# Performance work log

Measured on AMD Instinct MI355X. Metric: run time of the kernel, lower is better.

The kernel has to match this reference:

```python
import jax, jax.numpy as jnp
import numpy as np
from jax import lax

V, E, H, L, B, T = 32000, 300, 512, 17, 32, 256


def _lstm_dir(x, w_ih, w_hh, b_ih, b_hh):
    # x: [B,T,E]; torch gate order i,f,g,o stacked in 4H
    Bn = x.shape[0]
    xg = jnp.einsum('bte,ge->btg', x, w_ih) + b_ih + b_hh  # [B,T,4H]
    h0 = jnp.zeros((Bn, H), x.dtype)
    c0 = jnp.zeros((Bn, H), x.dtype)

    def step(carry, xg_t):
        h, c = carry
        g = xg_t + h @ w_hh.T
        i, f, gg, o = jnp.split(g, 4, axis=-1)
        i = jax.nn.sigmoid(i)
        f = jax.nn.sigmoid(f)
        gg = jnp.tanh(gg)
        o = jax.nn.sigmoid(o)
        c = f * c + i * gg
        h = o * jnp.tanh(c)
        return (h, c), h

    _, hs = lax.scan(step, (h0, c0), jnp.swapaxes(xg, 0, 1))
    return jnp.swapaxes(hs, 0, 1)  # [B,T,H]


def _forward(input_ids, labels, mask, emb, w_ih_f, w_hh_f, b_ih_f, b_hh_f,
             w_ih_b, w_hh_b, b_ih_b, b_hh_b, w_cls, b_cls,
             start_trans, end_trans, trans):
    x = emb[input_ids]                                   # [B,T,E]
    hf = _lstm_dir(x, w_ih_f, w_hh_f, b_ih_f, b_hh_f)
    hb = _lstm_dir(x[:, ::-1], w_ih_b, w_hh_b, b_ih_b, b_hh_b)[:, ::-1]
    h = jnp.concatenate([hf, hb], axis=-1)               # [B,T,2H]
    em = h @ w_cls.T + b_cls                             # [B,T,L] emissions

    # ---- CRF log-likelihood (torchcrf semantics), time-major ----
    em_t = jnp.swapaxes(em, 0, 1)                        # [T,B,L]
    tags = jnp.swapaxes(labels, 0, 1)                    # [T,B]
    m = jnp.swapaxes(mask, 0, 1).astype(em.dtype)        # [T,B]
    barange = jnp.arange(em.shape[0])

    # numerator: score of gold path
    score = start_trans[tags[0]] + em_t[0, barange, tags[0]]

    def num_step(s, inp):
        e_t, tp, tt, mt = inp
        return s + mt * (trans[tp, tt] + e_t[barange, tt]), None

    score, _ = lax.scan(num_step, score, (em_t[1:], tags[:-1], tags[1:], m[1:]))
    seq_ends = jnp.sum(m, axis=0).astype(jnp.int32) - 1
    last_tags = tags[seq_ends, barange]
    score = score + end_trans[last_tags]

    # denominator: forward algorithm (log partition)
    alpha = start_trans + em_t[0]                        # [B,L]

    def den_step(a, inp):
        e_t, mt = inp
        nxt = jax.nn.logsumexp(a[:, :, None] + trans[None, :, :] + e_t[:, None, :], axis=1)
        return jnp.where(mt[:, None] > 0, nxt, a), None

    alpha, _ = lax.scan(den_step, alpha, (em_t[1:], m[1:]))
    logZ = jax.nn.logsumexp(alpha + end_trans, axis=-1)

    llh = score - logZ                                   # [B]
    return -jnp.mean(llh)                                # reduction='mean', loss = -llh


def setup_inputs():
    key = jax.random.key(0)
    ks = jax.random.split(key, 16)
    s = 1.0 / np.sqrt(H)
    s2 = 1.0 / np.sqrt(2 * H)
    u = lambda k, shp, sc: jax.random.uniform(k, shp, jnp.float32, -sc, sc)
    emb = jax.random.normal(ks[0], (V, E), jnp.float32)
    emb = emb.at[0].set(0.0)  # padding_idx=0 row zeroed
    return {
        'input_ids': jax.random.randint(ks[1], (B, T), 0, V, jnp.int32),
        'labels': jax.random.randint(ks[2], (B, T), 0, L, jnp.int32),
        'mask': jnp.ones((B, T), bool),
        'emb': emb,
        'w_ih_f': u(ks[3], (4 * H, E), s), 'w_hh_f': u(ks[4], (4 * H, H), s),
        'b_ih_f': u(ks[5], (4 * H,), s), 'b_hh_f': u(ks[6], (4 * H,), s),
        'w_ih_b': u(ks[7], (4 * H, E), s), 'w_hh_b': u(ks[8], (4 * H, H), s),
        'b_ih_b': u(ks[9], (4 * H,), s), 'b_hh_b': u(ks[10], (4 * H,), s),
        'w_cls': u(ks[11], (L, 2 * H), s2), 'b_cls': u(ks[12], (L,), s2),
        'start_trans': u(ks[13], (L,), 0.1),
        'end_trans': u(ks[14], (L,), 0.1),
        'trans': u(ks[15], (L, L), 0.1),
    }


def reference(input_ids, labels, mask, emb, w_ih_f, w_hh_f, b_ih_f, b_hh_f,
              w_ih_b, w_hh_b, b_ih_b, b_hh_b, w_cls, b_cls,
              start_trans, end_trans, trans):
    return _forward(input_ids, labels, mask, emb, w_ih_f, w_hh_f, b_ih_f, b_hh_f,
                    w_ih_b, w_hh_b, b_ih_b, b_hh_b, w_cls, b_cls,
                    start_trans, end_trans, trans)
```

## Files before the change

### kernel.cpp

```cpp
#include <hip/hip_runtime.h>

#define TT 256
#define BB 32
#define HH 512
#define EE 300
#define LL 17
#define G4 2048

#define NGRP 16

using u16 = unsigned short;
using u32 = unsigned int;
using u64 = unsigned long long;

typedef _Float16 half8 __attribute__((ext_vector_type(8)));
typedef short bf16x8 __attribute__((ext_vector_type(8)));
typedef float f32x4 __attribute__((ext_vector_type(4)));

__device__ __forceinline__ u32 f2bf(float f) {
  u32 u = __float_as_uint(f);
  return (u + 0x7FFFu + ((u >> 16) & 1u)) >> 16;
}
__device__ __forceinline__ float bfbits2f(u32 lo) { return __uint_as_float(lo << 16); }

__device__ __forceinline__ u32 pkf16(float a, float b) {
  u16 lo = __builtin_bit_cast(u16, (_Float16)a);
  u16 hi = __builtin_bit_cast(u16, (_Float16)b);
  return (u32)lo | ((u32)hi << 16);
}
__device__ __forceinline__ float f16lo(u32 p) {
  return (float)__builtin_bit_cast(_Float16, (u16)(p & 0xFFFFu));
}
__device__ __forceinline__ float f16hi(u32 p) {
  return (float)__builtin_bit_cast(_Float16, (u16)(p >> 16));
}

#define RX __ATOMIC_RELAXED
#define SCA __HIP_MEMORY_SCOPE_AGENT

__global__ __launch_bounds__(256) void k_zero(u64* __restrict__ hx64) {
  int i = blockIdx.x * 256 + threadIdx.x;
  if (i < 2 * NGRP * 1024) hx64[i] = 0ull;
}

__global__ __launch_bounds__(256) void k_pack4(
    const float* __restrict__ whhf, const float* __restrict__ whhb,
    uint4* __restrict__ wpk2)
{
  int g = blockIdx.x * 256 + threadIdx.x;
  int l = g & 63;
  int kstep = (g >> 6) & 15;
  int t = (g >> 10) & 3;
  int js = (g >> 12) & 31;
  int dir = (g >> 17) & 1;
  int r = l & 15;
  int jl = 4 * t + (r >> 2), gate = r & 3;
  int grow = gate * 512 + js * 16 + jl;
  int k0 = kstep * 32 + (l >> 4) * 8;
  const float* wsrc = (dir ? whhb : whhf) + (long)grow * HH + k0;
  uint4 o;
  o.x = pkf16(wsrc[0], wsrc[1]);
  o.y = pkf16(wsrc[2], wsrc[3]);
  o.z = pkf16(wsrc[4], wsrc[5]);
  o.w = pkf16(wsrc[6], wsrc[7]);
  wpk2[g] = o;
}

__global__ __launch_bounds__(256) void k_input_gemm2(
    const int* __restrict__ ids, const float* __restrict__ emb,
    const float* __restrict__ wih_f, const float* __restrict__ wih_b,
    const float* __restrict__ bih_f, const float* __restrict__ bhh_f,
    const float* __restrict__ bih_b, const float* __restrict__ bhh_b,
    u16* __restrict__ xgf, u16* __restrict__ xgb)
{
  __shared__ u32 As[128 * 20];
  __shared__ u32 Bs[128 * 20];
  __shared__ int idl[128];

  const int tid = threadIdx.x;
  const int mb = blockIdx.x & 63;
  const int nb = blockIdx.x >> 6;
  const int m0 = mb * 128;
  const int dir = nb >> 4;
  const int gl0 = (nb & 15) * 128;
  const float* __restrict__ wih = dir ? wih_b : wih_f;

  if (tid < 128) {
    int tk = m0 + tid;
    idl[tid] = ids[(tk & 31) * TT + (tk >> 5)];
  }
  __syncthreads();

  const int w = tid >> 6, l = tid & 63;
  const int lr = l & 15, lq = l >> 4;
  const int sm = tid >> 1, shalf = tid & 1;

  f32x4 acc[2][8];
#pragma unroll
  for (int mi = 0; mi < 2; ++mi)
#pragma unroll
    for (int ni = 0; ni < 8; ++ni) acc[mi][ni] = (f32x4){0.f, 0.f, 0.f, 0.f};

  for (int kc = 0; kc < 10; ++kc) {
    const int kg = kc * 32 + shalf * 16;
    {
      const float* src = emb + (long)idl[sm] * EE;
      u32 pk[8];
#pragma unroll
      for (int j4 = 0; j4 < 4; ++j4) {
        int k = kg + 4 * j4;
        float f0, f1, f2, f3;
        if (k + 3 < EE) {
          float4 v = *(const float4*)(src + k);
          f0 = v.x; f1 = v.y; f2 = v.z; f3 = v.w;
        } else {
          f0 = (k < EE) ? src[k] : 0.f;
          f1 = (k + 1 < EE) ? src[k + 1] : 0.f;
          f2 = (k + 2 < EE) ? src[k + 2] : 0.f;
          f3 = (k + 3 < EE) ? src[k + 3] : 0.f;
        }
        pk[2 * j4] = f2bf(f0) | (f2bf(f1) << 16);
        pk[2 * j4 + 1] = f2bf(f2) | (f2bf(f3) << 16);
      }
      *(uint4*)&As[sm * 20 + shalf * 8] = make_uint4(pk[0], pk[1], pk[2], pk[3]);
      *(uint4*)&As[sm * 20 + shalf * 8 + 4] = make_uint4(pk[4], pk[5], pk[6], pk[7]);
    }
    {
      const float* src = wih + (long)(gl0 + sm) * EE;
      u32 pk[8];
#pragma unroll
      for (int j4 = 0; j4 < 4; ++j4) {
        int k = kg + 4 * j4;
        float f0, f1, f2, f3;
        if (k + 3 < EE) {
          float4 v = *(const float4*)(src + k);
          f0 = v.x; f1 = v.y; f2 = v.z; f3 = v.w;
        } else {
          f0 = (k < EE) ? src[k] : 0.f;
          f1 = (k + 1 < EE) ? src[k + 1] : 0.f;
          f2 = (k + 2 < EE) ? src[k + 2] : 0.f;
          f3 = (k + 3 < EE) ? src[k + 3] : 0.f;
        }
        pk[2 * j4] = f2bf(f0) | (f2bf(f1) << 16);
        pk[2 * j4 + 1] = f2bf(f2) | (f2bf(f3) << 16);
      }
      *(uint4*)&Bs[sm * 20 + shalf * 8] = make_uint4(pk[0], pk[1], pk[2], pk[3]);
      *(uint4*)&Bs[sm * 20 + shalf * 8 + 4] = make_uint4(pk[4], pk[5], pk[6], pk[7]);
    }
    __syncthreads();

    bf16x8 Af[2];
#pragma unroll
    for (int mi = 0; mi < 2; ++mi)
      Af[mi] = __builtin_bit_cast(
          bf16x8, *(const uint4*)&As[(w * 32 + mi * 16 + lr) * 20 + lq * 4]);
#pragma unroll
    for (int ni = 0; ni < 8; ++ni) {
      bf16x8 Bf = __builtin_bit_cast(
          bf16x8, *(const uint4*)&Bs[(ni * 16 + lr) * 20 + lq * 4]);
      acc[0][ni] = __builtin_amdgcn_mfma_f32_16x16x32_bf16(Af[0], Bf, acc[0][ni], 0, 0, 0);
      acc[1][ni] = __builtin_amdgcn_mfma_f32_16x16x32_bf16(Af[1], Bf, acc[1][ni], 0, 0, 0);
    }
    __syncthreads();
  }

  const float* __restrict__ bih = dir ? bih_b : bih_f;
  const float* __restrict__ bhh = dir ? bhh_b : bhh_f;
  u16* __restrict__ xg = dir ? xgb : xgf;
  float bias[8];
#pragma unroll
  for (int ni = 0; ni < 8; ++ni) {
    int g = gl0 + ni * 16 + lr;
    bias[ni] = bih[g] + bhh[g];
  }
#pragma unroll
  for (int mi = 0; mi < 2; ++mi)
#pragma unroll
    for (int ni = 0; ni < 8; ++ni)
#pragma unroll
      for (int r = 0; r < 4; ++r) {
        int tk = m0 + w * 32 + mi * 16 + lq * 4 + r;
        xg[(long)tk * G4 + gl0 + ni * 16 + lr] = (u16)f2bf(acc[mi][ni][r] + bias[ni]);
      }
}

__global__ __launch_bounds__(256, 1) void k_lstm15(
    const u16* __restrict__ xgf, const u16* __restrict__ xgb,
    const uint4* __restrict__ wpk2,
    u64* __restrict__ hx64,
    u32* __restrict__ hsf32, u32* __restrict__ hsb32)
{
  __shared__ uint4 cB[2][2][256];

  const int tid = threadIdx.x;
  const int bx = blockIdx.x;
  const int bg = bx & 7;
  const int js = bx >> 3;

  const int dh = tid >> 7;
  const int u = tid & 127;
  const int wv = (tid >> 6) & 1;
  const int l = tid & 63;
  const int grp = dh * 8 + bg;

  const u16* __restrict__ xg = dh ? xgb : xgf;
  u32* __restrict__ hs32 = dh ? hsb32 : hsf32;

  const int ub = l & 15;
  const bool ubv = ub < 4;
  const int bread = (l >> 4) * 4 + (ub & 3);
  const int jl0 = 8 * wv + (l >> 4);

  half8 A0[16], A1[16];
  {
    const uint4* ap = wpk2 + ((long)dh << 17) + ((long)js << 12) +
                      ((2 * wv) << 10) + l;
#pragma unroll
    for (int ks = 0; ks < 16; ++ks) {
      A0[ks] = __builtin_bit_cast(half8, ap[ks << 6]);
      A1[ks] = __builtin_bit_cast(half8, ap[1024 + (ks << 6)]);
    }
  }

  {
    uint4* c = &cB[0][0][0];
    for (int i = tid; i < 1024; i += 256) c[i] = make_uint4(0u, 0u, 0u, 0u);
  }
  __syncthreads();

  float cs0 = 0.f, cs1 = 0.f;

  for (int s = 0; s < TT; ++s) {
    const int tok = dh ? (TT - 1 - s) : s;

    u32 xq0[4] = {0, 0, 0, 0}, xq1[4] = {0, 0, 0, 0};
    if (ubv) {
      const u16* p = xg + ((long)(tok * BB + bg * 4 + ub) << 11) + js * 16 + jl0;
      xq0[0] = p[0]; xq0[1] = p[512]; xq0[2] = p[1024]; xq0[3] = p[1536];
      const u16* q = p + 4;
      xq1[0] = q[0]; xq1[1] = q[512]; xq1[2] = q[1024]; xq1[3] = q[1536];
    }

    if (s > 0) {
      const u64* hp = hx64 + ((long)(((s - 1) & 1) * NGRP + grp) << 10) + 8 * u;
      const u32 want = (u32)s;
      u64 v0, v1, v2, v3, v4, v5, v6, v7;
      for (;;) {
        v0 = __hip_atomic_load(hp + 0, RX, SCA);
        v1 = __hip_atomic_load(hp + 1, RX, SCA);
        v2 = __hip_atomic_load(hp + 2, RX, SCA);
        v3 = __hip_atomic_load(hp + 3, RX, SCA);
        v4 = __hip_atomic_load(hp + 4, RX, SCA);
        v5 = __hip_atomic_load(hp + 5, RX, SCA);
        v6 = __hip_atomic_load(hp + 6, RX, SCA);
        v7 = __hip_atomic_load(hp + 7, RX, SCA);
        bool ok = ((u32)(v0 >> 32) == want) & ((u32)(v1 >> 32) == want) &
                  ((u32)(v2 >> 32) == want) & ((u32)(v3 >> 32) == want) &
                  ((u32)(v4 >> 32) == want) & ((u32)(v5 >> 32) == want) &
                  ((u32)(v6 >> 32) == want) & ((u32)(v7 >> 32) == want);
        if (ok) break;
        __builtin_amdgcn_s_sleep(1);
      }
      const int par = s & 1;
      const int i0 = 2 * u, i1 = 2 * u + 1;
      const int pk0 = (i0 >> 2) & 15;
      const int e0 = (pk0 * 16 + (i0 & 3) * 4 + (i0 >> 6)) ^ (pk0 & 7);
      const int e1 = (pk0 * 16 + (i1 & 3) * 4 + (i1 >> 6)) ^ (pk0 & 7);
      cB[dh][par][e0] = make_uint4((u32)v0, (u32)v1, (u32)v2, (u32)v3);
      cB[dh][par][e1] = make_uint4((u32)v4, (u32)v5, (u32)v6, (u32)v7);
    }
    __syncthreads();

    f32x4 acc0 = {0.f, 0.f, 0.f, 0.f}, acc1 = {0.f, 0.f, 0.f, 0.f};
    {
      const uint4* cb = &cB[dh][s & 1][0];
#pragma unroll
      for (int ks = 0; ks < 16; ++ks) {
        half8 B = __builtin_bit_cast(half8, cb[(ks * 16 + bread) ^ (ks & 7)]);
        acc0 = __builtin_amdgcn_mfma_f32_16x16x32_f16(A0[ks], B, acc0, 0, 0, 0);
        acc1 = __builtin_amdgcn_mfma_f32_16x16x32_f16(A1[ks], B, acc1, 0, 0, 0);
      }
    }

    {
      float hv = 0.f;
      if (ubv) {
        float y0 = acc0[0] + bfbits2f(xq0[0]);
        float y1 = acc0[1] + bfbits2f(xq0[1]);
        float y2 = acc0[2] + bfbits2f(xq0[2]);
        float y3 = acc0[3] + bfbits2f(xq0[3]);
        float i_ = 1.f / (1.f + __expf(-y0));
        float f_ = 1.f / (1.f + __expf(-y1));
        float gc = fminf(fmaxf(y2, -15.f), 15.f);
        float eg = __expf(2.f * gc);
        float g_ = (eg - 1.f) / (eg + 1.f);
        float o_ = 1.f / (1.f + __expf(-y3));
        cs0 = f_ * cs0 + i_ * g_;
        float cc = fminf(fmaxf(cs0, -15.f), 15.f);
        float ec = __expf(2.f * cc);
        hv = o_ * (ec - 1.f) / (ec + 1.f);
      }
      float hnb = __shfl_down(hv, 16);
      if (ubv && !((l >> 4) & 1)) {
        u32 pr = pkf16(hv, hnb);
        int jp = js * 8 + 4 * wv + ((l >> 4) >> 1);
        __hip_atomic_store(hs32 + ((long)(tok * BB + bg * 4 + ub) << 8) + jp,
                           pr, RX, SCA);
        u64 v = ((u64)(u32)(s + 1) << 32) | (u64)pr;
        __hip_atomic_store(hx64 + ((long)((s & 1) * NGRP + grp) << 10) +
                               ub * 256 + jp, v, RX, SCA);
      }
    }
    {
      float hv = 0.f;
      if (ubv) {
        float y0 = acc1[0] + bfbits2f(xq1[0]);
        float y1 = acc1[1] + bfbits2f(xq1[1]);
        float y2 = acc1[2] + bfbits2f(xq1[2]);
        float y3 = acc1[3] + bfbits2f(xq1[3]);
        float i_ = 1.f / (1.f + __expf(-y0));
        float f_ = 1.f / (1.f + __expf(-y1));
        float gc = fminf(fmaxf(y2, -15.f), 15.f);
        float eg = __expf(2.f * gc);
        float g_ = (eg - 1.f) / (eg + 1.f);
        float o_ = 1.f / (1.f + __expf(-y3));
        cs1 = f_ * cs1 + i_ * g_;
        float cc = fminf(fmaxf(cs1, -15.f), 15.f);
        float ec = __expf(2.f * cc);
        hv = o_ * (ec - 1.f) / (ec + 1.f);
      }
      float hnb = __shfl_down(hv, 16);
      if (ubv && !((l >> 4) & 1)) {
        u32 pr = pkf16(hv, hnb);
        int jp = js * 8 + 4 * wv + 2 + ((l >> 4) >> 1);
        __hip_atomic_store(hs32 + ((long)(tok * BB + bg * 4 + ub) << 8) + jp,
                           pr, RX, SCA);
        u64 v = ((u64)(u32)(s + 1) << 32) | (u64)pr;
        __hip_atomic_store(hx64 + ((long)((s & 1) * NGRP + grp) << 10) +
                               ub * 256 + jp, v, RX, SCA);
      }
    }
  }
}

__global__ __launch_bounds__(128) void k_cls(
    const u32* __restrict__ hsf32, const u32* __restrict__ hsb32,
    const float* __restrict__ wcls, const float* __restrict__ bcls,
    float* __restrict__ em)
{
  __shared__ float h_l[1024];
  __shared__ float part[17][4];
  const int tk = blockIdx.x;
  const int tid = threadIdx.x;

  {
    uint2 vf = ((const uint2*)(hsf32 + (long)tk * 256))[tid];
    uint2 vb = ((const uint2*)(hsb32 + (long)tk * 256))[tid];
    h_l[4 * tid + 0] = f16lo(vf.x); h_l[4 * tid + 1] = f16hi(vf.x);
    h_l[4 * tid + 2] = f16lo(vf.y); h_l[4 * tid + 3] = f16hi(vf.y);
    h_l[512 + 4 * tid + 0] = f16lo(vb.x); h_l[512 + 4 * tid + 1] = f16hi(vb.x);
    h_l[512 + 4 * tid + 2] = f16lo(vb.y); h_l[512 + 4 * tid + 3] = f16hi(vb.y);
  }
  __syncthreads();

  if (tid < 68) {
    const int ll = tid >> 2, kq = tid & 3;
    const float4* wr = (const float4*)(wcls + (long)ll * 1024 + kq * 256);
    const float4* hr = (const float4*)(h_l + kq * 256);
    float sum = 0.f;
#pragma unroll 4
    for (int i = 0; i < 64; ++i) {
      float4 a = hr[i]; float4 wv = wr[i];
      sum += a.x * wv.x + a.y * wv.y + a.z * wv.z + a.w * wv.w;
    }
    part[ll][kq] = sum;
  }
  __syncthreads();
  if (tid < LL) {
    float v = bcls[tid] + part[tid][0] + part[tid][1] + part[tid][2] + part[tid][3];
    int t = tk >> 5, b = tk & 31;
    em[(long)t * (BB * LL) + b * LL + tid] = v;
  }
}

__global__ __launch_bounds__(64) void k_crf2(
    const float* __restrict__ em, const int* __restrict__ labels,
    const float* __restrict__ st, const float* __restrict__ et,
    const float* __restrict__ trans, float* __restrict__ llh)
{
  __shared__ float tr[LL * LL];
  __shared__ float scp[LL];
  const int b = blockIdx.x;
  const int l = threadIdx.x;

  for (int i = l; i < LL * LL; i += 64) tr[i] = trans[i];
  __syncthreads();

  const bool act = l < LL;
  float trc[LL];
#pragma unroll
  for (int i = 0; i < LL; ++i) trc[i] = act ? tr[i * LL + l] : 0.f;

  float a = act ? (st[l] + em[b * LL + l]) : -1e30f;

  for (int t = 1; t < TT; ++t) {
    float emv = act ? em[(long)t * (BB * LL) + b * LL + l] : 0.f;
    float tmp[LL];
#pragma unroll
    for (int i = 0; i < LL; ++i) tmp[i] = __shfl(a, i) + trc[i];
    float m = tmp[0];
#pragma unroll
    for (int i = 1; i < LL; ++i) m = fmaxf(m, tmp[i]);
    float s = 0.f;
#pragma unroll
    for (int i = 0; i < LL; ++i) s += __expf(tmp[i] - m);
    if (act) a = m + __logf(s) + emv;
  }

  float fin[LL];
#pragma unroll
  for (int i = 0; i < LL; ++i) fin[i] = __shfl(a, i);

  float np = 0.f;
  if (act) {
    for (int t = 1 + l; t < TT; t += LL) {
      int tp = labels[b * TT + t - 1], tc = labels[b * TT + t];
      np += tr[tp * LL + tc] + em[(long)t * (BB * LL) + b * LL + tc];
    }
    scp[l] = np;
  }
  __syncthreads();

  if (l == 0) {
    float mz = -1e30f;
#pragma unroll
    for (int i = 0; i < LL; ++i) { fin[i] += et[i]; mz = fmaxf(mz, fin[i]); }
    float sz = 0.f;
#pragma unroll
    for (int i = 0; i < LL; ++i) sz += __expf(fin[i] - mz);
    float logz = mz + __logf(sz);

    float score = 0.f;
#pragma unroll
    for (int i = 0; i < LL; ++i) score += scp[i];
    int t0 = labels[b * TT], tl = labels[b * TT + TT - 1];
    score += st[t0] + em[b * LL + t0] + et[tl];

    llh[b] = score - logz;
  }
}

__global__ __launch_bounds__(64) void k_fin(const float* __restrict__ llh,
                                            float* __restrict__ out) {
  int l = threadIdx.x;
  float v = (l < BB) ? llh[l] : 0.f;
#pragma unroll
  for (int m = 16; m >= 1; m >>= 1) v += __shfl_xor(v, m);
  if (l == 0) out[0] = -v / (float)BB;
}

extern "C" void kernel_launch(void* const* d_in, const int* in_sizes, int n_in,
                              void* d_out, int out_size, void* d_ws, size_t ws_size,
                              hipStream_t stream) {
  (void)in_sizes; (void)n_in; (void)out_size; (void)ws_size;

  const int* ids     = (const int*)d_in[0];
  const int* labels  = (const int*)d_in[1];
  const float* emb   = (const float*)d_in[3];
  const float* wih_f = (const float*)d_in[4];
  const float* whh_f = (const float*)d_in[5];
  const float* bih_f = (const float*)d_in[6];
  const float* bhh_f = (const float*)d_in[7];
  const float* wih_b = (const float*)d_in[8];
  const float* whh_b = (const float*)d_in[9];
  const float* bih_b = (const float*)d_in[10];
  const float* bhh_b = (const float*)d_in[11];
  const float* wcls  = (const float*)d_in[12];
  const float* bcls  = (const float*)d_in[13];
  const float* st    = (const float*)d_in[14];
  const float* et    = (const float*)d_in[15];
  const float* tr    = (const float*)d_in[16];

  char* ws = (char*)d_ws;
  size_t off = 0;
  auto carve = [&](size_t bytes) -> void* {
    void* p = ws + off;
    off += (bytes + 255) & ~(size_t)255;
    return p;
  };
  u16* xgf    = (u16*)carve((size_t)TT * BB * G4 * sizeof(u16));
  u16* xgb    = (u16*)carve((size_t)TT * BB * G4 * sizeof(u16));
  uint4* wpk2 = (uint4*)carve((size_t)262144 * sizeof(uint4));
  u32* hsf32  = (u32*)carve((size_t)TT * BB * 256 * sizeof(u32));
  u32* hsb32  = (u32*)carve((size_t)TT * BB * 256 * sizeof(u32));
  float* em   = (float*)carve((size_t)TT * BB * LL * sizeof(float));
  u64* hx64   = (u64*)carve((size_t)2 * NGRP * 1024 * sizeof(u64));
  float* llh  = (float*)carve((size_t)BB * sizeof(float));

  hipLaunchKernelGGL(k_zero, dim3(128), dim3(256), 0, stream, hx64);

  hipLaunchKernelGGL(k_pack4, dim3(1024), dim3(256), 0, stream,
                     whh_f, whh_b, wpk2);

  hipLaunchKernelGGL(k_input_gemm2, dim3(2048), dim3(256), 0, stream,
                     ids, emb, wih_f, wih_b, bih_f, bhh_f, bih_b, bhh_b, xgf, xgb);

  {
    void* args[] = {(void*)&xgf, (void*)&xgb, (void*)&wpk2,
                    (void*)&hx64, (void*)&hsf32, (void*)&hsb32};
    hipLaunchCooperativeKernel((void*)k_lstm15, dim3(256), dim3(256), args,
                               0, stream);
  }

  hipLaunchKernelGGL(k_cls, dim3(TT * BB), dim3(128), 0, stream,
                     hsf32, hsb32, wcls, bcls, em);

  hipLaunchKernelGGL(k_crf2, dim3(BB), dim3(64), 0, stream,
                     em, labels, st, et, tr, llh);

  hipLaunchKernelGGL(k_fin, dim3(1), dim3(64), 0, stream, llh, (float*)d_out);
}
```

Measured before the change: 933.0 us.

## Pre-pack GEMM operands to bf16 and run classifier projection on MFMA

Adds a packing kernel that gathers embeddings and converts the input weights to padded bf16 buffers, and also packs the classifier weights into an f16 MFMA fragment layout. The input GEMM then copies pre-packed data straight into shared memory instead of converting fp32 in the inner loop. The classifier changes from 8192 scalar-dot-product blocks to 64 blocks using MFMA 16x16x32 f16 tiles. The cost is an extra launch and an extra trip through global memory for the packed buffers. The recurrent LSTM kernel, which likely dominates, is unchanged.

```diff
diff --git a/kernel.cpp b/kernel.cpp
--- a/kernel.cpp
+++ b/kernel.cpp
@@ -66,16 +66,60 @@
   wpk2[g] = o;
 }
 
-__global__ __launch_bounds__(256) void k_input_gemm2(
+#define PX_X 1310720L
+#define PX_W 655360L
+__global__ __launch_bounds__(256) void k_packx(
     const int* __restrict__ ids, const float* __restrict__ emb,
-    const float* __restrict__ wih_f, const float* __restrict__ wih_b,
+    const float* __restrict__ wihf_, const float* __restrict__ wihb_,
+    const float* __restrict__ wcls,
+    u32* __restrict__ xemb, u32* __restrict__ wihb2,
+    uint4* __restrict__ wclsf)
+{
+  long idx = (long)blockIdx.x * 256 + threadIdx.x;
+  if (idx < PX_X) {
+    int tk = (int)(idx / 160), kc = (int)(idx % 160);
+    int t = tk >> 5, b = tk & 31;
+    int id = ids[b * TT + t];
+    const float* src = emb + (long)id * EE + 2 * kc;
+    float f0 = (2 * kc < EE) ? src[0] : 0.f;
+    float f1 = (2 * kc + 1 < EE) ? src[1] : 0.f;
+    xemb[idx] = f2bf(f0) | (f2bf(f1) << 16);
+  } else if (idx < PX_X + PX_W) {
+    long j = idx - PX_X;
+    int dir = j >= (PX_W / 2);
+    long jj = dir ? j - (PX_W / 2) : j;
+    int g = (int)(jj / 160), kc = (int)(jj % 160);
+    const float* w = (dir ? wihb_ : wihf_) + (long)g * EE + 2 * kc;
+    float f0 = (2 * kc < EE) ? w[0] : 0.f;
+    float f1 = (2 * kc + 1 < EE) ? w[1] : 0.f;
+    wihb2[j] = f2bf(f0) | (f2bf(f1) << 16);
+  } else {
+    long j = idx - PX_X - PX_W;
+    if (j < 4096) {
+      int l = (int)(j & 63), ks = (int)((j >> 6) & 31), nt = (int)(j >> 11);
+      int ll = nt * 16 + (l & 15);
+      int k0 = ks * 32 + (l >> 4) * 8;
+      uint4 o = make_uint4(0u, 0u, 0u, 0u);
+      if (ll < LL) {
+        const float* w = wcls + (long)ll * 1024 + k0;
+        o.x = pkf16(w[0], w[1]);
+        o.y = pkf16(w[2], w[3]);
+        o.z = pkf16(w[4], w[5]);
+        o.w = pkf16(w[6], w[7]);
+      }
+      wclsf[j] = o;
+    }
+  }
+}
+
+__global__ __launch_bounds__(256) void k_input_gemm3(
+    const u32* __restrict__ xemb, const u32* __restrict__ wihb2,
     const float* __restrict__ bih_f, const float* __restrict__ bhh_f,
     const float* __restrict__ bih_b, const float* __restrict__ bhh_b,
     u16* __restrict__ xgf, u16* __restrict__ xgb)
 {
   __shared__ u32 As[128 * 20];
   __shared__ u32 Bs[128 * 20];
-  __shared__ int idl[128];
 
   const int tid = threadIdx.x;
   const int mb = blockIdx.x & 63;
@@ -83,18 +127,13 @@
   const int m0 = mb * 128;
   const int dir = nb >> 4;
   const int gl0 = (nb & 15) * 128;
-  const float* __restrict__ wih = dir ? wih_b : wih_f;
-
-  if (tid < 128) {
-    int tk = m0 + tid;
-    idl[tid] = ids[(tk & 31) * TT + (tk >> 5)];
-  }
-  __syncthreads();
 
   const int w = tid >> 6, l = tid & 63;
   const int lr = l & 15, lq = l >> 4;
   const int sm = tid >> 1, shalf = tid & 1;
 
+  const u32* __restrict__ wsrc = wihb2 + (long)dir * (PX_W / 2);
+
   f32x4 acc[2][8];
 #pragma unroll
   for (int mi = 0; mi < 2; ++mi)
@@ -102,50 +141,13 @@
     for (int ni = 0; ni < 8; ++ni) acc[mi][ni] = (f32x4){0.f, 0.f, 0.f, 0.f};
 
   for (int kc = 0; kc < 10; ++kc) {
-    const int kg = kc * 32 + shalf * 16;
     {
-      const float* src = emb + (long)idl[sm] * EE;
-      u32 pk[8];
-#pragma unroll
-      for (int j4 = 0; j4 < 4; ++j4) {
-        int k = kg + 4 * j4;
-        float f0, f1, f2, f3;
-        if (k + 3 < EE) {
-          float4 v = *(const float4*)(src + k);
-          f0 = v.x; f1 = v.y; f2 = v.z; f3 = v.w;
-        } else {
-          f0 = (k < EE) ? src[k] : 0.f;
-          f1 = (k + 1 < EE) ? src[k + 1] : 0.f;
-          f2 = (k + 2 < EE) ? src[k + 2] : 0.f;
-          f3 = (k + 3 < EE) ? src[k + 3] : 0.f;
-        }
-        pk[2 * j4] = f2bf(f0) | (f2bf(f1) << 16);
-        pk[2 * j4 + 1] = f2bf(f2) | (f2bf(f3) << 16);
-      }
-      *(uint4*)&As[sm * 20 + shalf * 8] = make_uint4(pk[0], pk[1], pk[2], pk[3]);
-      *(uint4*)&As[sm * 20 + shalf * 8 + 4] = make_uint4(pk[4], pk[5], pk[6], pk[7]);
-    }
-    {
-      const float* src = wih + (long)(gl0 + sm) * EE;
-      u32 pk[8];
-#pragma unroll
-      for (int j4 = 0; j4 < 4; ++j4) {
-        int k = kg + 4 * j4;
-        float f0, f1, f2, f3;
-        if (k + 3 < EE) {
-          float4 v = *(const float4*)(src + k);
-          f0 = v.x; f1 = v.y; f2 = v.z; f3 = v.w;
-        } else {
-          f0 = (k < EE) ? src[k] : 0.f;
-          f1 = (k + 1 < EE) ? src[k + 1] : 0.f;
-          f2 = (k + 2 < EE) ? src[k + 2] : 0.f;
-          f3 = (k + 3 < EE) ? src[k + 3] : 0.f;
-        }
-        pk[2 * j4] = f2bf(f0) | (f2bf(f1) << 16);
-        pk[2 * j4 + 1] = f2bf(f2) | (f2bf(f3) << 16);
-      }
-      *(uint4*)&Bs[sm * 20 + shalf * 8] = make_uint4(pk[0], pk[1], pk[2], pk[3]);
-      *(uint4*)&Bs[sm * 20 + shalf * 8 + 4] = make_uint4(pk[4], pk[5], pk[6], pk[7]);
+      const u32* sa = xemb + (long)(m0 + sm) * 160 + kc * 16 + shalf * 8;
+      *(uint4*)&As[sm * 20 + shalf * 8] = *(const uint4*)sa;
+      *(uint4*)&As[sm * 20 + shalf * 8 + 4] = *(const uint4*)(sa + 4);
+      const u32* sb = wsrc + (long)(gl0 + sm) * 160 + kc * 16 + shalf * 8;
+      *(uint4*)&Bs[sm * 20 + shalf * 8] = *(const uint4*)sb;
+      *(uint4*)&Bs[sm * 20 + shalf * 8 + 4] = *(const uint4*)(sb + 4);
     }
     __syncthreads();
 
@@ -343,43 +345,51 @@
   }
 }
 
-__global__ __launch_bounds__(128) void k_cls(
+__global__ __launch_bounds__(256) void k_cls3(
     const u32* __restrict__ hsf32, const u32* __restrict__ hsb32,
-    const float* __restrict__ wcls, const float* __restrict__ bcls,
+    const uint4* __restrict__ wclsf, const float* __restrict__ bcls,
     float* __restrict__ em)
 {
-  __shared__ float h_l[1024];
-  __shared__ float part[17][4];
-  const int tk = blockIdx.x;
   const int tid = threadIdx.x;
-
-  {
-    uint2 vf = ((const uint2*)(hsf32 + (long)tk * 256))[tid];
-    uint2 vb = ((const uint2*)(hsb32 + (long)tk * 256))[tid];
-    h_l[4 * tid + 0] = f16lo(vf.x); h_l[4 * tid + 1] = f16hi(vf.x);
-    h_l[4 * tid + 2] = f16lo(vf.y); h_l[4 * tid + 3] = f16hi(vf.y);
-    h_l[512 + 4 * tid + 0] = f16lo(vb.x); h_l[512 + 4 * tid + 1] = f16hi(vb.x);
-    h_l[512 + 4 * tid + 2] = f16lo(vb.y); h_l[512 + 4 * tid + 3] = f16hi(vb.y);
-  }
-  __syncthreads();
-
-  if (tid < 68) {
-    const int ll = tid >> 2, kq = tid & 3;
-    const float4* wr = (const float4*)(wcls + (long)ll * 1024 + kq * 256);
-    const float4* hr = (const float4*)(h_l + kq * 256);
-    float sum = 0.f;
+  const int tk0 = blockIdx.x * 128;
+  const int w = tid >> 6, l = tid & 63;
+  const int lr = l & 15, lq = l >> 4;
+
+  f32x4 acc[2][2];
+#pragma unroll
+  for (int mi = 0; mi < 2; ++mi)
+#pragma unroll
+    for (int nt = 0; nt < 2; ++nt) acc[mi][nt] = (f32x4){0.f, 0.f, 0.f, 0.f};
+
 #pragma unroll 4
-    for (int i = 0; i < 64; ++i) {
-      float4 a = hr[i]; float4 wv = wr[i];
-      sum += a.x * wv.x + a.y * wv.y + a.z * wv.z + a.w * wv.w;
-    }
-    part[ll][kq] = sum;
-  }
-  __syncthreads();
-  if (tid < LL) {
-    float v = bcls[tid] + part[tid][0] + part[tid][1] + part[tid][2] + part[tid][3];
-    int t = tk >> 5, b = tk & 31;
-    em[(long)t * (BB * LL) + b * LL + tid] = v;
+  for (int ks = 0; ks < 32; ++ks) {
+    half8 B0 = __builtin_bit_cast(half8, wclsf[ks * 64 + l]);
+    half8 B1 = __builtin_bit_cast(half8, wclsf[2048 + ks * 64 + l]);
+    const u32* __restrict__ hsrc = (ks < 16) ? hsf32 : hsb32;
+    const int ks2 = ks & 15;
+#pragma unroll
+    for (int mi = 0; mi < 2; ++mi) {
+      int tk = tk0 + w * 32 + mi * 16 + lr;
+      uint4 av = *(const uint4*)(hsrc + (long)tk * 256 + ks2 * 16 + lq * 4);
+      half8 A = __builtin_bit_cast(half8, av);
+      acc[mi][0] = __builtin_amdgcn_mfma_f32_16x16x32_f16(A, B0, acc[mi][0], 0, 0, 0);
+      acc[mi][1] = __builtin_amdgcn_mfma_f32_16x16x32_f16(A, B1, acc[mi][1], 0, 0, 0);
+    }
+  }
+
+#pragma unroll
+  for (int nt = 0; nt < 2; ++nt) {
+    int ll = nt * 16 + lr;
+    if (ll < LL) {
+      float bb = bcls[ll];
+#pragma unroll
+      for (int mi = 0; mi < 2; ++mi)
+#pragma unroll
+        for (int r = 0; r < 4; ++r) {
+          int tk = tk0 + w * 32 + mi * 16 + lq * 4 + r;
+          em[(long)tk * LL + ll] = acc[mi][nt][r] + bb;
+        }
+    }
   }
 }
 
@@ -404,7 +414,7 @@
   float a = act ? (st[l] + em[b * LL + l]) : -1e30f;
 
   for (int t = 1; t < TT; ++t) {
-    float emv = act ? em[(long)t * (BB * LL) + b * LL + l] : 0.f;
+    float emv = act ? em[(long)(t * BB + b) * LL + l] : 0.f;
     float tmp[LL];
 #pragma unroll
     for (int i = 0; i < LL; ++i) tmp[i] = __shfl(a, i) + trc[i];
@@ -425,7 +435,7 @@
   if (act) {
     for (int t = 1 + l; t < TT; t += LL) {
       int tp = labels[b * TT + t - 1], tc = labels[b * TT + t];
-      np += tr[tp * LL + tc] + em[(long)t * (BB * LL) + b * LL + tc];
+      np += tr[tp * LL + tc] + em[(long)(t * BB + b) * LL + tc];
     }
     scp[l] = np;
   }
@@ -444,7 +454,7 @@
 #pragma unroll
     for (int i = 0; i < LL; ++i) score += scp[i];
     int t0 = labels[b * TT], tl = labels[b * TT + TT - 1];
-    score += st[t0] + em[b * LL + t0] + et[tl];
+    score += st[t0] + em[(long)b * LL + t0] + et[tl];
 
     llh[b] = score - logz;
   }
@@ -496,14 +506,20 @@
   float* em   = (float*)carve((size_t)TT * BB * LL * sizeof(float));
   u64* hx64   = (u64*)carve((size_t)2 * NGRP * 1024 * sizeof(u64));
   float* llh  = (float*)carve((size_t)BB * sizeof(float));
+  u32* xemb   = (u32*)carve((size_t)PX_X * sizeof(u32));
+  u32* wihb2  = (u32*)carve((size_t)PX_W * sizeof(u32));
+  uint4* wclsf = (uint4*)carve((size_t)4096 * sizeof(uint4));
 
   hipLaunchKernelGGL(k_zero, dim3(128), dim3(256), 0, stream, hx64);
 
   hipLaunchKernelGGL(k_pack4, dim3(1024), dim3(256), 0, stream,
                      whh_f, whh_b, wpk2);
 
-  hipLaunchKernelGGL(k_input_gemm2, dim3(2048), dim3(256), 0, stream,
-                     ids, emb, wih_f, wih_b, bih_f, bhh_f, bih_b, bhh_b, xgf, xgb);
+  hipLaunchKernelGGL(k_packx, dim3(7696), dim3(256), 0, stream,
+                     ids, emb, wih_f, wih_b, wcls, xemb, wihb2, wclsf);
+
+  hipLaunchKernelGGL(k_input_gemm3, dim3(2048), dim3(256), 0, stream,
+                     xemb, wihb2, bih_f, bhh_f, bih_b, bhh_b, xgf, xgb);
 
   {
     void* args[] = {(void*)&xgf, (void*)&xgb, (void*)&wpk2,
@@ -512,8 +528,8 @@
                                0, stream);
   }
 
-  hipLaunchKernelGGL(k_cls, dim3(TT * BB), dim3(128), 0, stream,
-                     hsf32, hsb32, wcls, bcls, em);
+  hipLaunchKernelGGL(k_cls3, dim3(64), dim3(256), 0, stream,
+                     hsf32, hsb32, wclsf, bcls, em);
 
   hipLaunchKernelGGL(k_crf2, dim3(BB), dim3(64), 0, stream,
                      em, labels, st, et, tr, llh);
```

Result: faster. 862.9 us (-7.5%).
